# Kernel tuning notes

Measured on AMD Instinct MI355X. Metric: run time of the kernel, lower is better.

Reference implementation:

```python
import jax, jax.numpy as jnp
import numpy as np

B, T, C = 8, 2048, 1024   # batch, seq_len, n_embd
H = 128                   # head_size

def setup_inputs() -> dict:
    key = jax.random.key(0)
    kx, kk, kq, kv = jax.random.split(key, 4)
    scale = 1.0 / np.sqrt(C)
    return {
        "x": jax.random.normal(kx, (B, T, C), dtype=jnp.float32),
        "Wk": jax.random.normal(kk, (C, H), dtype=jnp.float32) * scale,
        "Wq": jax.random.normal(kq, (C, H), dtype=jnp.float32) * scale,
        "Wv": jax.random.normal(kv, (C, H), dtype=jnp.float32) * scale,
    }

def reference(x, Wk, Wq, Wv):
    # k,q,v: [B,T,H]
    k = x @ Wk
    q = x @ Wq
    v = x @ Wv
    # NOTE: original scales by C**-0.5 (n_embd), not head_size**-0.5
    wei = jnp.einsum("bth,bsh->bts", q, k) * (x.shape[-1] ** -0.5)  # [B,T,T]
    wei = jax.nn.softmax(wei, axis=-1)  # no causal mask in the source module
    # dropout = 0.0 -> identity
    out = jnp.einsum("bts,bsh->bth", wei, v)  # [B,T,H]
    return out
```

## Files before the change

kernel.cpp:

```cpp
#include <hip/hip_runtime.h>
#include <hip/hip_bf16.h>
#include <stdint.h>
#include <stddef.h>

#define NB 8
#define NT 2048
#define NC 1024
#define NH 128

typedef float f32x4 __attribute__((ext_vector_type(4)));
typedef short bf16x8 __attribute__((ext_vector_type(8)));
typedef short bf16x4 __attribute__((ext_vector_type(4)));

__device__ __forceinline__ unsigned short f2bf(float f) {
    union { float f; uint32_t u; } v; v.f = f;
    uint32_t u = v.u;
    u += 0x7fffu + ((u >> 16) & 1u);
    return (unsigned short)(u >> 16);
}

__device__ __forceinline__ void gld16(const void* gp, void* lp) {
    __builtin_amdgcn_global_load_lds(
        (const __attribute__((address_space(1))) unsigned int*)gp,
        (__attribute__((address_space(3))) unsigned int*)lp, 16, 0, 0);
}


__global__ __launch_bounds__(256) void cast_w_kernel(const float* __restrict__ Wq,
                                                     const float* __restrict__ Wk,
                                                     const float* __restrict__ Wv,
                                                     unsigned short* __restrict__ Wtf) {
    int gid  = blockIdx.x * 256 + threadIdx.x;
    int lane = gid & 63;
    int fs   = gid >> 6;
    int kb   = fs & 31;
    int g    = fs >> 5;
    int w    = g >> 3;
    int g16  = g & 7;
    int quad = lane >> 4;
    int l16  = lane & 15;
    const float* src = (w == 0) ? Wq : ((w == 1) ? Wk : Wv);
    int n = g16 * 16 + l16;
    bf16x8 o;
#pragma unroll
    for (int j = 0; j < 8; ++j)
        o[j] = (short)f2bf(src[(size_t)(kb * 32 + quad * 8 + j) * 128 + n]);
    *(bf16x8*)(Wtf + (size_t)gid * 8) = o;
}

#define CS2 392

__global__ __launch_bounds__(512, 2) void proj_kernel(const float* __restrict__ x,
                                                      const unsigned short* __restrict__ Wtf,
                                                      unsigned short* __restrict__ Qf,
                                                      unsigned short* __restrict__ Kf,
                                                      unsigned short* __restrict__ Vf) {
    __shared__ __align__(16) unsigned short wbuf[4][24 * 512];
    __shared__ __align__(16) unsigned short abuf[2][64 * 128];

    const int tid  = threadIdx.x;
    const int wave = tid >> 6;
    const int lane = tid & 63;
    const int quad = lane >> 4;
    const int l16  = lane & 15;
    const int bidx = blockIdx.x;
    const int rowbase = bidx * 64;
    const int b    = bidx >> 5;
    const int mh   = wave & 1;
    const int nq   = wave >> 1;

    const int arow = wave * 8 + (lane >> 3);
    const float* axp = x + (size_t)(rowbase + arow) * NC;
    const int aswz = (arow & 7) << 3;
    const int rswz = (l16 & 7) << 3;

    float4 aS[2][4];
    f32x4 acc0[6] = {};
    f32x4 acc1[6] = {};

#define STAGE(KB, BI) { _Pragma("unroll") \
    for (int i_ = 0; i_ < 3; ++i_) { \
        const int g_ = wave * 3 + i_; \
        gld16(Wtf + ((size_t)(g_ * 32 + (KB)) * 512) + lane * 8, &wbuf[BI][g_ * 512]); } }

#define LOADA(C, S) { _Pragma("unroll") \
    for (int i_ = 0; i_ < 4; ++i_) \
        aS[S][i_] = *(const float4*)(axp + (C) * 128 + i_ * 32 + (lane & 7) * 4); }

#define DSWRITE(C, S) { _Pragma("unroll") \
    for (int i_ = 0; i_ < 4; ++i_) { \
        bf16x4 t_; \
        t_[0] = (short)f2bf(aS[S][i_].x); t_[1] = (short)f2bf(aS[S][i_].y); \
        t_[2] = (short)f2bf(aS[S][i_].z); t_[3] = (short)f2bf(aS[S][i_].w); \
        *(bf16x4*)(&abuf[(C) & 1][arow * 128 + ((i_ * 32 + (lane & 7) * 4) ^ aswz)]) = t_; } }

#define BARW(N) { asm volatile("s_waitcnt vmcnt(" #N ") lgkmcnt(0)" ::: "memory"); \
                  __builtin_amdgcn_s_barrier(); }

#define TICK(K, CUR) { \
    const unsigned short* ab_ = abuf[((K) >> 2) & 1]; \
    const int t2_ = ((K) & 3) * 32 + quad * 8; \
    bf16x8 af0 = *(const bf16x8*)(ab_ + (mh * 32 + l16) * 128 + (t2_ ^ rswz)); \
    bf16x8 af1 = *(const bf16x8*)(ab_ + (mh * 32 + 16 + l16) * 128 + (t2_ ^ rswz)); \
    _Pragma("unroll") \
    for (int i_ = 0; i_ < 6; ++i_) { \
        bf16x8 wf_ = *(const bf16x8*)(&wbuf[CUR][(nq * 6 + i_) * 512 + lane * 8]); \
        acc0[i_] = __builtin_amdgcn_mfma_f32_16x16x32_bf16(af0, wf_, acc0[i_], 0, 0, 0); \
        acc1[i_] = __builtin_amdgcn_mfma_f32_16x16x32_bf16(af1, wf_, acc1[i_], 0, 0, 0); } }

    LOADA(0, 0); LOADA(1, 1);
    STAGE(0, 0); STAGE(1, 1); STAGE(2, 2);
    asm volatile("s_waitcnt vmcnt(13)" ::: "memory");
    DSWRITE(0, 0);
    BARW(6);

    for (int c = 0; c < 6; ++c) {
        const int k0 = c * 4;
        LOADA(c + 2, c & 1);
        STAGE(k0 + 3, 3); TICK(k0 + 0, 0); BARW(10);
        STAGE(k0 + 4, 0); TICK(k0 + 1, 1); BARW(10);
        STAGE(k0 + 5, 1); TICK(k0 + 2, 2); BARW(6);
        STAGE(k0 + 6, 2); TICK(k0 + 3, 3); DSWRITE(c + 1, (c + 1) & 1); BARW(6);
    }
    STAGE(27, 3); TICK(24, 0); BARW(6);
    STAGE(28, 0); TICK(25, 1); BARW(6);
    STAGE(29, 1); TICK(26, 2); BARW(6);
    STAGE(30, 2); TICK(27, 3); DSWRITE(7, 1); BARW(6);
    STAGE(31, 3); TICK(28, 0); BARW(6);
    TICK(29, 1); BARW(3);
    TICK(30, 2); BARW(0);
    TICK(31, 3);
    asm volatile("s_waitcnt vmcnt(0) lgkmcnt(0)" ::: "memory");
    __builtin_amdgcn_s_barrier();

    unsigned short* cs = (unsigned short*)wbuf;
#pragma unroll
    for (int i = 0; i < 6; ++i) {
#pragma unroll
        for (int r = 0; r < 4; ++r) {
            cs[(mh * 32 +  0 + quad * 4 + r) * CS2 + nq * 96 + i * 16 + l16] = f2bf(acc0[i][r]);
            cs[(mh * 32 + 16 + quad * 4 + r) * CS2 + nq * 96 + i * 16 + l16] = f2bf(acc1[i][r]);
        }
    }
    __syncthreads();

    const int ibase = (rowbase & (NT - 1)) >> 4;
    const int tc    = (rowbase & (NT - 1)) >> 5;
    unsigned short* qdst = Qf + (size_t)b * (NT * NH);
    unsigned short* kdst = Kf + (size_t)b * (NT * NH);
    unsigned short* vdst = Vf + (size_t)b * (NT * NH);

#pragma unroll
    for (int j = 0; j < 6; ++j) {
        const int s = wave * 6 + j;
        if (s < 32) {
            const int isK = s >> 4;
            const int t   = s & 15;
            const int m   = t >> 2;
            const int ks  = t & 3;
            unsigned short* dst = isK ? kdst : qdst;
            bf16x8 v = *(const bf16x8*)(&cs[(m * 16 + l16) * CS2 + isK * 128 + ks * 32 + quad * 8]);
            *(bf16x8*)(dst + ((size_t)((ibase + m) * 4 + ks) * 64 + lane) * 8) = v;
        } else {
            const int vv = s - 32;
            const int nt = vv >> 1;
            const int cc = vv & 1;
            bf16x8 v;
#pragma unroll
            for (int jj = 0; jj < 8; ++jj)
                v[jj] = (short)cs[(cc * 32 + quad * 8 + jj) * CS2 + 256 + nt * 16 + l16];
            *(bf16x8*)(vdst + ((size_t)(nt * 64 + tc + cc) * 64 + lane) * 8) = v;
        }
    }

#undef TICK
#undef BARW
#undef DSWRITE
#undef LOADA
#undef STAGE
}

#define AKBUF(BI) (smem + (size_t)(BI) * 8192)
#define AVBUF(BI) (smem + 24576 + (size_t)(BI) * 8192)

__global__ __launch_bounds__(512, 1) void attn_kernel(const unsigned short* __restrict__ Qf,
                                                      const unsigned short* __restrict__ Kf,
                                                      const unsigned short* __restrict__ Vf,
                                                      float* __restrict__ out) {
    __shared__ __align__(16) unsigned short smem[6 * 16 * 512];
    __shared__ __align__(16) unsigned short p_grp[4][32 * 40];
    __shared__ float sl[8][32];

    const int tid  = threadIdx.x;
    const int wave = tid >> 6;
    const int lane = tid & 63;
    const int quad = lane >> 4;
    const int l16  = lane & 15;
    const int bid  = blockIdx.x;
    const int b    = bid & 7;
    const int iqg  = bid >> 3;
    const int mh   = wave & 1;
    const int kh   = (wave >> 1) & 1;
    const int nh   = wave >> 2;
    const int kq   = kh * 2 + nh;

    const unsigned short* qfp = Qf + (size_t)b * (NT * NH);
    const unsigned short* kfp = Kf + (size_t)b * (NT * NH);
    const unsigned short* vfp = Vf + (size_t)b * (NT * NH);
    unsigned short* pg = p_grp[mh * 2 + kh];

    const int iq0 = iqg * 4 + mh * 2;
    bf16x8 qf0[4], qf1[4];
#pragma unroll
    for (int ks = 0; ks < 4; ++ks) {
        qf0[ks] = *(const bf16x8*)(qfp + ((size_t)((iq0 + 0) * 4 + ks) * 64 + lane) * 8);
        qf1[ks] = *(const bf16x8*)(qfp + ((size_t)((iq0 + 1) * 4 + ks) * 64 + lane) * 8);
    }

    auto stage = [&](int j, int bi) {
#pragma unroll
        for (int i = 0; i < 4; ++i) {
            const int fid = wave * 4 + i;
            if (fid < 16) {
                gld16(kfp + ((size_t)(j * 16 + fid) * 512) + lane * 8, AKBUF(bi) + fid * 512);
            } else {
                const int s  = fid - 16;
                const int nt = s >> 1;
                const int c  = s & 1;
                gld16(vfp + ((size_t)(nt * 64 + j * 2 + c) * 512) + lane * 8, AVBUF(bi) + s * 512);
            }
        }
    };

    stage(0, 0);
    stage(1, 1);
    asm volatile("s_waitcnt vmcnt(4)" ::: "memory");
    __builtin_amdgcn_s_barrier();

    f32x4 O0[4] = {}, O1[4] = {};
    float lsum0[4] = {0.f, 0.f, 0.f, 0.f};
    float lsum1[4] = {0.f, 0.f, 0.f, 0.f};
    const float scl2 = 0.03125f * 1.44269504088896340736f;

    for (int j = 0; j < 32; ++j) {
        const int cur = j - (j / 3) * 3;
        const int nxt = (j + 2 >= 3 * ((j + 2) / 3)) ? (j + 2) - 3 * ((j + 2) / 3) : 0;
        if (j < 30) stage(j + 2, nxt);
        const unsigned short* kb = AKBUF(cur);
        const unsigned short* vb = AVBUF(cur);

        f32x4 S0 = {}, S1 = {};
#pragma unroll
        for (int ks = 0; ks < 4; ++ks) {
            bf16x8 kf = *(const bf16x8*)(kb + (kq * 4 + ks) * 512 + lane * 8);
            S0 = __builtin_amdgcn_mfma_f32_16x16x32_bf16(qf0[ks], kf, S0, 0, 0, 0);
            S1 = __builtin_amdgcn_mfma_f32_16x16x32_bf16(qf1[ks], kf, S1, 0, 0, 0);
        }

#pragma unroll
        for (int r = 0; r < 4; ++r) {
            float p0 = __builtin_amdgcn_exp2f(S0[r] * scl2);
            float p1 = __builtin_amdgcn_exp2f(S1[r] * scl2);
            lsum0[r] += p0;
            lsum1[r] += p1;
            pg[(quad * 4 + r) * 40 + nh * 16 + l16]        = f2bf(p0);
            pg[(16 + quad * 4 + r) * 40 + nh * 16 + l16]   = f2bf(p1);
        }

        asm volatile("s_waitcnt lgkmcnt(0)" ::: "memory");
        __builtin_amdgcn_s_barrier();

        bf16x8 pf0 = *(const bf16x8*)(&pg[l16 * 40 + quad * 8]);
        bf16x8 pf1 = *(const bf16x8*)(&pg[(16 + l16) * 40 + quad * 8]);
#pragma unroll
        for (int i = 0; i < 4; ++i) {
            const int nt = nh * 4 + i;
            bf16x8 vf = *(const bf16x8*)(vb + (nt * 2 + kh) * 512 + lane * 8);
            O0[i] = __builtin_amdgcn_mfma_f32_16x16x32_bf16(pf0, vf, O0[i], 0, 0, 0);
            O1[i] = __builtin_amdgcn_mfma_f32_16x16x32_bf16(pf1, vf, O1[i], 0, 0, 0);
        }

        if (j < 30) {
            asm volatile("s_waitcnt vmcnt(4) lgkmcnt(0)" ::: "memory");
        } else {
            asm volatile("s_waitcnt vmcnt(0) lgkmcnt(0)" ::: "memory");
        }
        __builtin_amdgcn_s_barrier();
    }

#pragma unroll
    for (int msk = 1; msk <= 8; msk <<= 1) {
#pragma unroll
        for (int r = 0; r < 4; ++r) {
            lsum0[r] += __shfl_xor(lsum0[r], msk, 64);
            lsum1[r] += __shfl_xor(lsum1[r], msk, 64);
        }
    }
    if (l16 == 0) {
#pragma unroll
        for (int r = 0; r < 4; ++r) {
            sl[wave][quad * 4 + r]      = lsum0[r];
            sl[wave][16 + quad * 4 + r] = lsum1[r];
        }
    }
    __syncthreads();

    float* od = (float*)smem;
    const int g = nh * 2 + mh;
    if (kh == 1) {
        float* myod = od + (size_t)g * 32 * 68;
#pragma unroll
        for (int i = 0; i < 4; ++i) {
#pragma unroll
            for (int r = 0; r < 4; ++r) {
                myod[(quad * 4 + r) * 68 + i * 16 + l16]      = O0[i][r];
                myod[(16 + quad * 4 + r) * 68 + i * 16 + l16] = O1[i][r];
            }
        }
    }
    __syncthreads();

    if (kh == 0) {
        float inv0[4], inv1[4];
#pragma unroll
        for (int r = 0; r < 4; ++r) {
            inv0[r] = 1.0f / (sl[mh][quad * 4 + r] + sl[2 + mh][quad * 4 + r] +
                              sl[4 + mh][quad * 4 + r] + sl[6 + mh][quad * 4 + r]);
            inv1[r] = 1.0f / (sl[mh][16 + quad * 4 + r] + sl[2 + mh][16 + quad * 4 + r] +
                              sl[4 + mh][16 + quad * 4 + r] + sl[6 + mh][16 + quad * 4 + r]);
        }
        const float* pod = od + (size_t)g * 32 * 68;
        float* orow = out + ((size_t)b * NT + iqg * 64 + mh * 32) * NH + nh * 64;
#pragma unroll
        for (int i = 0; i < 4; ++i) {
#pragma unroll
            for (int r = 0; r < 4; ++r) {
                float v0 = O0[i][r] + pod[(quad * 4 + r) * 68 + i * 16 + l16];
                float v1 = O1[i][r] + pod[(16 + quad * 4 + r) * 68 + i * 16 + l16];
                orow[(quad * 4 + r) * NH + i * 16 + l16]      = v0 * inv0[r];
                orow[(16 + quad * 4 + r) * NH + i * 16 + l16] = v1 * inv1[r];
            }
        }
    }
}

#undef AKBUF
#undef AVBUF

extern "C" void kernel_launch(void* const* d_in, const int* in_sizes, int n_in,
                              void* d_out, int out_size, void* d_ws, size_t ws_size,
                              hipStream_t stream) {
    const float* x  = (const float*)d_in[0];
    const float* Wk = (const float*)d_in[1];
    const float* Wq = (const float*)d_in[2];
    const float* Wv = (const float*)d_in[3];
    float* out = (float*)d_out;

    char* ws = (char*)d_ws;
    unsigned short* Qf  = (unsigned short*)(ws);
    unsigned short* Kf  = (unsigned short*)(ws + 4194304);
    unsigned short* Vf  = (unsigned short*)(ws + 8388608);
    unsigned short* Wtf = (unsigned short*)(ws + 12582912);

    cast_w_kernel<<<192, 256, 0, stream>>>(Wq, Wk, Wv, Wtf);
    proj_kernel<<<256, 512, 0, stream>>>(x, Wtf, Qf, Kf, Vf);
    attn_kernel<<<256, 512, 0, stream>>>(Qf, Kf, Vf, out);
}
```

Before: 155.4 us.

## Keep P in registers via transposed QK^T and 16x16x16 PV MFMAs

```diff
diff --git a/kernel.cpp b/kernel.cpp
--- a/kernel.cpp
+++ b/kernel.cpp
@@ -23,6 +23,19 @@
     __builtin_amdgcn_global_load_lds(
         (const __attribute__((address_space(1))) unsigned int*)gp,
         (__attribute__((address_space(3))) unsigned int*)lp, 16, 0, 0);
+}
+
+__device__ __forceinline__ f32x4 mfma16(bf16x4 a, bf16x4 b, f32x4 c) {
+#if __has_builtin(__builtin_amdgcn_mfma_f32_16x16x16_bf16)
+    return __builtin_amdgcn_mfma_f32_16x16x16_bf16(a, b, c, 0, 0, 0);
+#elif __has_builtin(__builtin_amdgcn_mfma_f32_16x16x16bf16_1k)
+    return __builtin_amdgcn_mfma_f32_16x16x16bf16_1k(a, b, c, 0, 0, 0);
+#else
+    f32x4 d;
+    asm volatile("v_mfma_f32_16x16x16_bf16 %0, %1, %2, %3"
+                 : "=v"(d) : "v"(a), "v"(b), "v"(c));
+    return d;
+#endif
 }
 
 
@@ -145,7 +158,6 @@
     __syncthreads();
 
     const int ibase = (rowbase & (NT - 1)) >> 4;
-    const int tc    = (rowbase & (NT - 1)) >> 5;
     unsigned short* qdst = Qf + (size_t)b * (NT * NH);
     unsigned short* kdst = Kf + (size_t)b * (NT * NH);
     unsigned short* vdst = Vf + (size_t)b * (NT * NH);
@@ -164,12 +176,16 @@
         } else {
             const int vv = s - 32;
             const int nt = vv >> 1;
-            const int cc = vv & 1;
-            bf16x8 v;
-#pragma unroll
-            for (int jj = 0; jj < 8; ++jj)
-                v[jj] = (short)cs[(cc * 32 + quad * 8 + jj) * CS2 + 256 + nt * 16 + l16];
-            *(bf16x8*)(vdst + ((size_t)(nt * 64 + tc + cc) * 64 + lane) * 8) = v;
+            const int pp = vv & 1;
+#pragma unroll
+            for (int ff = 0; ff < 2; ++ff) {
+                const int t4 = pp * 2 + ff;
+                bf16x4 v;
+#pragma unroll
+                for (int jj = 0; jj < 4; ++jj)
+                    v[jj] = (short)cs[(t4 * 16 + quad * 4 + jj) * CS2 + 256 + nt * 16 + l16];
+                *(bf16x4*)(vdst + (size_t)(nt * 128 + ibase + t4) * 256 + lane * 4) = v;
+            }
         }
     }
 
@@ -180,15 +196,14 @@
 #undef STAGE
 }
 
-#define AKBUF(BI) (smem + (size_t)(BI) * 8192)
-#define AVBUF(BI) (smem + 24576 + (size_t)(BI) * 8192)
+#define AKBUF(BI) (smem + (size_t)(BI) * 16384)
+#define AVBUF(BI) (smem + (size_t)(BI) * 16384 + 8192)
 
 __global__ __launch_bounds__(512, 1) void attn_kernel(const unsigned short* __restrict__ Qf,
                                                       const unsigned short* __restrict__ Kf,
                                                       const unsigned short* __restrict__ Vf,
                                                       float* __restrict__ out) {
-    __shared__ __align__(16) unsigned short smem[6 * 16 * 512];
-    __shared__ __align__(16) unsigned short p_grp[4][32 * 40];
+    __shared__ __align__(16) unsigned short smem[3 * 16384];
     __shared__ float sl[8][32];
 
     const int tid  = threadIdx.x;
@@ -200,14 +215,11 @@
     const int b    = bid & 7;
     const int iqg  = bid >> 3;
     const int mh   = wave & 1;
-    const int kh   = (wave >> 1) & 1;
-    const int nh   = wave >> 2;
-    const int kq   = kh * 2 + nh;
+    const int kq   = wave >> 1;
 
     const unsigned short* qfp = Qf + (size_t)b * (NT * NH);
     const unsigned short* kfp = Kf + (size_t)b * (NT * NH);
     const unsigned short* vfp = Vf + (size_t)b * (NT * NH);
-    unsigned short* pg = p_grp[mh * 2 + kh];
 
     const int iq0 = iqg * 4 + mh * 2;
     bf16x8 qf0[4], qf1[4];
@@ -220,14 +232,15 @@
     auto stage = [&](int j, int bi) {
 #pragma unroll
         for (int i = 0; i < 4; ++i) {
-            const int fid = wave * 4 + i;
-            if (fid < 16) {
+            if (wave < 4) {
+                const int fid = wave * 4 + i;
                 gld16(kfp + ((size_t)(j * 16 + fid) * 512) + lane * 8, AKBUF(bi) + fid * 512);
             } else {
-                const int s  = fid - 16;
-                const int nt = s >> 1;
-                const int c  = s & 1;
-                gld16(vfp + ((size_t)(nt * 64 + j * 2 + c) * 512) + lane * 8, AVBUF(bi) + s * 512);
+                const int sid = (wave - 4) * 4 + i;
+                const int nt = sid >> 1;
+                const int pp = sid & 1;
+                gld16(vfp + ((size_t)(nt * 128 + j * 4 + pp * 2) * 256) + lane * 8,
+                      AVBUF(bi) + (nt * 4 + pp * 2) * 256);
             }
         }
     };
@@ -237,15 +250,14 @@
     asm volatile("s_waitcnt vmcnt(4)" ::: "memory");
     __builtin_amdgcn_s_barrier();
 
-    f32x4 O0[4] = {}, O1[4] = {};
-    float lsum0[4] = {0.f, 0.f, 0.f, 0.f};
-    float lsum1[4] = {0.f, 0.f, 0.f, 0.f};
+    f32x4 O0[8] = {}, O1[8] = {};
+    float ls0 = 0.f, ls1 = 0.f;
     const float scl2 = 0.03125f * 1.44269504088896340736f;
 
+    int cur = 0;
     for (int j = 0; j < 32; ++j) {
-        const int cur = j - (j / 3) * 3;
-        const int nxt = (j + 2 >= 3 * ((j + 2) / 3)) ? (j + 2) - 3 * ((j + 2) / 3) : 0;
-        if (j < 30) stage(j + 2, nxt);
+        const int stb = (cur >= 1) ? cur - 1 : 2;
+        if (j < 30) stage(j + 2, stb);
         const unsigned short* kb = AKBUF(cur);
         const unsigned short* vb = AVBUF(cur);
 
@@ -253,31 +265,26 @@
 #pragma unroll
         for (int ks = 0; ks < 4; ++ks) {
             bf16x8 kf = *(const bf16x8*)(kb + (kq * 4 + ks) * 512 + lane * 8);
-            S0 = __builtin_amdgcn_mfma_f32_16x16x32_bf16(qf0[ks], kf, S0, 0, 0, 0);
-            S1 = __builtin_amdgcn_mfma_f32_16x16x32_bf16(qf1[ks], kf, S1, 0, 0, 0);
-        }
-
+            S0 = __builtin_amdgcn_mfma_f32_16x16x32_bf16(kf, qf0[ks], S0, 0, 0, 0);
+            S1 = __builtin_amdgcn_mfma_f32_16x16x32_bf16(kf, qf1[ks], S1, 0, 0, 0);
+        }
+
+        bf16x4 pf0, pf1;
 #pragma unroll
         for (int r = 0; r < 4; ++r) {
             float p0 = __builtin_amdgcn_exp2f(S0[r] * scl2);
             float p1 = __builtin_amdgcn_exp2f(S1[r] * scl2);
-            lsum0[r] += p0;
-            lsum1[r] += p1;
-            pg[(quad * 4 + r) * 40 + nh * 16 + l16]        = f2bf(p0);
-            pg[(16 + quad * 4 + r) * 40 + nh * 16 + l16]   = f2bf(p1);
-        }
-
-        asm volatile("s_waitcnt lgkmcnt(0)" ::: "memory");
-        __builtin_amdgcn_s_barrier();
-
-        bf16x8 pf0 = *(const bf16x8*)(&pg[l16 * 40 + quad * 8]);
-        bf16x8 pf1 = *(const bf16x8*)(&pg[(16 + l16) * 40 + quad * 8]);
-#pragma unroll
-        for (int i = 0; i < 4; ++i) {
-            const int nt = nh * 4 + i;
-            bf16x8 vf = *(const bf16x8*)(vb + (nt * 2 + kh) * 512 + lane * 8);
-            O0[i] = __builtin_amdgcn_mfma_f32_16x16x32_bf16(pf0, vf, O0[i], 0, 0, 0);
-            O1[i] = __builtin_amdgcn_mfma_f32_16x16x32_bf16(pf1, vf, O1[i], 0, 0, 0);
+            ls0 += p0;
+            ls1 += p1;
+            pf0[r] = (short)f2bf(p0);
+            pf1[r] = (short)f2bf(p1);
+        }
+
+#pragma unroll
+        for (int nt = 0; nt < 8; ++nt) {
+            bf16x4 vf = *(const bf16x4*)(vb + (nt * 4 + kq) * 256 + lane * 4);
+            O0[nt] = mfma16(pf0, vf, O0[nt]);
+            O1[nt] = mfma16(pf1, vf, O1[nt]);
         }
 
         if (j < 30) {
@@ -286,59 +293,76 @@
             asm volatile("s_waitcnt vmcnt(0) lgkmcnt(0)" ::: "memory");
         }
         __builtin_amdgcn_s_barrier();
-    }
-
-#pragma unroll
-    for (int msk = 1; msk <= 8; msk <<= 1) {
+        cur = (cur >= 2) ? 0 : cur + 1;
+    }
+
+    ls0 += __shfl_xor(ls0, 16, 64);
+    ls0 += __shfl_xor(ls0, 32, 64);
+    ls1 += __shfl_xor(ls1, 16, 64);
+    ls1 += __shfl_xor(ls1, 32, 64);
+    if (quad == 0) {
+        sl[wave][l16]      = ls0;
+        sl[wave][16 + l16] = ls1;
+    }
+
+    float* od = (float*)smem;
+    if (kq >= 2) {
+        float* myod = od + (size_t)((kq - 2) * 2 + mh) * 32 * 132;
+#pragma unroll
+        for (int nt = 0; nt < 8; ++nt) {
+#pragma unroll
+            for (int r = 0; r < 4; ++r) {
+                myod[(quad * 4 + r) * 132 + nt * 16 + l16]      = O0[nt][r];
+                myod[(16 + quad * 4 + r) * 132 + nt * 16 + l16] = O1[nt][r];
+            }
+        }
+    }
+    __syncthreads();
+    if (kq < 2) {
+        const float* pod = od + (size_t)(kq * 2 + mh) * 32 * 132;
+#pragma unroll
+        for (int nt = 0; nt < 8; ++nt) {
+#pragma unroll
+            for (int r = 0; r < 4; ++r) {
+                O0[nt][r] += pod[(quad * 4 + r) * 132 + nt * 16 + l16];
+                O1[nt][r] += pod[(16 + quad * 4 + r) * 132 + nt * 16 + l16];
+            }
+        }
+    }
+    __syncthreads();
+    if (kq == 1) {
+        float* myod = od + (size_t)mh * 32 * 132;
+#pragma unroll
+        for (int nt = 0; nt < 8; ++nt) {
+#pragma unroll
+            for (int r = 0; r < 4; ++r) {
+                myod[(quad * 4 + r) * 132 + nt * 16 + l16]      = O0[nt][r];
+                myod[(16 + quad * 4 + r) * 132 + nt * 16 + l16] = O1[nt][r];
+            }
+        }
+    }
+    __syncthreads();
+
+    if (kq == 0) {
+        float inv0[4], inv1[4];
 #pragma unroll
         for (int r = 0; r < 4; ++r) {
-            lsum0[r] += __shfl_xor(lsum0[r], msk, 64);
-            lsum1[r] += __shfl_xor(lsum1[r], msk, 64);
-        }
-    }
-    if (l16 == 0) {
-#pragma unroll
-        for (int r = 0; r < 4; ++r) {
-            sl[wave][quad * 4 + r]      = lsum0[r];
-            sl[wave][16 + quad * 4 + r] = lsum1[r];
-        }
-    }
-    __syncthreads();
-
-    float* od = (float*)smem;
-    const int g = nh * 2 + mh;
-    if (kh == 1) {
-        float* myod = od + (size_t)g * 32 * 68;
-#pragma unroll
-        for (int i = 0; i < 4; ++i) {
+            const int rr = quad * 4 + r;
+            inv0[r] = 1.0f / (sl[mh][rr] + sl[2 + mh][rr] +
+                              sl[4 + mh][rr] + sl[6 + mh][rr]);
+            inv1[r] = 1.0f / (sl[mh][16 + rr] + sl[2 + mh][16 + rr] +
+                              sl[4 + mh][16 + rr] + sl[6 + mh][16 + rr]);
+        }
+        const float* pod = od + (size_t)mh * 32 * 132;
+        float* orow = out + ((size_t)b * NT + iqg * 64 + mh * 32) * NH;
+#pragma unroll
+        for (int nt = 0; nt < 8; ++nt) {
 #pragma unroll
             for (int r = 0; r < 4; ++r) {
-                myod[(quad * 4 + r) * 68 + i * 16 + l16]      = O0[i][r];
-                myod[(16 + quad * 4 + r) * 68 + i * 16 + l16] = O1[i][r];
-            }
-        }
-    }
-    __syncthreads();
-
-    if (kh == 0) {
-        float inv0[4], inv1[4];
-#pragma unroll
-        for (int r = 0; r < 4; ++r) {
-            inv0[r] = 1.0f / (sl[mh][quad * 4 + r] + sl[2 + mh][quad * 4 + r] +
-                              sl[4 + mh][quad * 4 + r] + sl[6 + mh][quad * 4 + r]);
-            inv1[r] = 1.0f / (sl[mh][16 + quad * 4 + r] + sl[2 + mh][16 + quad * 4 + r] +
-                              sl[4 + mh][16 + quad * 4 + r] + sl[6 + mh][16 + quad * 4 + r]);
-        }
-        const float* pod = od + (size_t)g * 32 * 68;
-        float* orow = out + ((size_t)b * NT + iqg * 64 + mh * 32) * NH + nh * 64;
-#pragma unroll
-        for (int i = 0; i < 4; ++i) {
-#pragma unroll
-            for (int r = 0; r < 4; ++r) {
-                float v0 = O0[i][r] + pod[(quad * 4 + r) * 68 + i * 16 + l16];
-                float v1 = O1[i][r] + pod[(16 + quad * 4 + r) * 68 + i * 16 + l16];
-                orow[(quad * 4 + r) * NH + i * 16 + l16]      = v0 * inv0[r];
-                orow[(16 + quad * 4 + r) * NH + i * 16 + l16] = v1 * inv1[r];
+                float v0 = O0[nt][r] + pod[(quad * 4 + r) * 132 + nt * 16 + l16];
+                float v1 = O1[nt][r] + pod[(16 + quad * 4 + r) * 132 + nt * 16 + l16];
+                orow[(quad * 4 + r) * NH + nt * 16 + l16]      = v0 * inv0[r];
+                orow[(16 + quad * 4 + r) * NH + nt * 16 + l16] = v1 * inv1[r];
             }
         }
     }
```

New measurement: 149.7 us. 3.7% less time.
